# Performance work log

Measured on AMD Instinct MI355X. Metric: run time of the kernel, lower is better.

Reference implementation:

```python
import jax, jax.numpy as jnp
import numpy as np

WS = 8
HEADS = 12


def _dwconv(x, w, b):
    # x: (N, C, H, W); w: (C, 1, 3, 3) depthwise, zero pad 1
    y = jax.lax.conv_general_dilated(
        x, w, window_strides=(1, 1), padding=((1, 1), (1, 1)),
        dimension_numbers=("NCHW", "OIHW", "NCHW"), feature_group_count=x.shape[1])
    return y + b[None, :, None, None]


def _sepconv(x, dw, db, pw, pb):
    y = _dwconv(x, dw, db)
    # pointwise 1x1 conv: (N,C,H,W) x (O,C) -> (N,O,H,W)
    return jnp.einsum("nchw,oc->nohw", y, pw) + pb[None, :, None, None]


def _rel_pos_index(ws):
    coords = np.stack(np.meshgrid(np.arange(ws), np.arange(ws), indexing="ij"))  # (2, ws, ws)
    cf = coords.reshape(2, -1)
    rel = cf[:, :, None] - cf[:, None, :]          # (2, ws*ws, ws*ws)
    rel = rel.transpose(1, 2, 0).copy()
    rel[..., 0] += ws - 1
    rel[..., 1] += ws - 1
    rel[..., 0] *= 2 * ws - 1
    return rel.sum(-1)                             # (ws*ws, ws*ws)


def setup_inputs() -> dict:
    key = jax.random.key(0)
    ks = jax.random.split(key, 16)
    B, T, C, H, W = 2, 1, 384, 192, 192
    s = 0.02
    inp = {
        "vid": jax.random.normal(ks[0], (B, T, C, H, W), jnp.float32),
        "qd_w": jax.random.normal(ks[1], (C, 1, 3, 3), jnp.float32) * s,
        "qd_b": jnp.zeros((C,), jnp.float32),
        "qp_w": jax.random.normal(ks[2], (C, C), jnp.float32) * s,
        "qp_b": jnp.zeros((C,), jnp.float32),
        "kd_w": jax.random.normal(ks[3], (C, 1, 3, 3), jnp.float32) * s,
        "kd_b": jnp.zeros((C,), jnp.float32),
        "kp_w": jax.random.normal(ks[4], (C, C), jnp.float32) * s,
        "kp_b": jnp.zeros((C,), jnp.float32),
        "vd_w": jax.random.normal(ks[5], (C, 1, 3, 3), jnp.float32) * s,
        "vd_b": jnp.zeros((C,), jnp.float32),
        "vp_w": jax.random.normal(ks[6], (C, C), jnp.float32) * s,
        "vp_b": jnp.zeros((C,), jnp.float32),
        "rpb_table": jax.random.normal(ks[7], ((2 * WS - 1) ** 2, HEADS), jnp.float32) * s,
        "proj_w": jax.random.normal(ks[8], (C, C), jnp.float32) * s,
        "proj_b": jnp.zeros((C,), jnp.float32),
    }
    return inp


def reference(vid, qd_w, qd_b, qp_w, qp_b, kd_w, kd_b, kp_w, kp_b,
              vd_w, vd_b, vp_w, vp_b, rpb_table, proj_w, proj_b):
    B, T, C, H, W = vid.shape
    heads, ws = HEADS, WS
    hd = C // heads
    scale = hd ** -0.5
    x = vid.reshape(B * T, C, H, W)

    q = _sepconv(x, qd_w, qd_b, qp_w, qp_b) * scale
    k = _sepconv(x, kd_w, kd_b, kp_w, kp_b)
    v = _sepconv(x, vd_w, vd_b, vp_w, vp_b)

    nh, nw = H // ws, W // ws

    def win(z):  # (N, C, H, W) -> (N*nh*nw, heads, ws*ws, hd)
        N = z.shape[0]
        z = z.reshape(N, heads, hd, nh, ws, nw, ws)
        z = z.transpose(0, 3, 5, 1, 4, 6, 2)  # N, nh, nw, heads, ws, ws, hd
        return z.reshape(N * nh * nw, heads, ws * ws, hd)

    qw, kw, vw = win(q), win(k), win(v)

    # product search within window (dists = q . k), rel-pos bias softmax
    attn = jnp.einsum("nhqd,nhkd->nhqk", qw, kw)
    rp_idx = _rel_pos_index(ws)  # static (64, 64)
    bias = rpb_table[rp_idx.reshape(-1)].reshape(ws * ws, ws * ws, heads)
    bias = bias.transpose(2, 0, 1)  # (heads, 64, 64)
    attn = jax.nn.softmax(attn + bias[None], axis=-1)

    # weighted patch sum (ps=1 -> pixels)
    out = jnp.einsum("nhqk,nhkd->nhqd", attn, vw)  # (N*nh*nw, heads, ws*ws, hd)

    # un-window, merge heads into (h c) channel order, then token projection
    out = out.reshape(B * T, nh, nw, heads, ws, ws, hd)
    out = out.transpose(0, 1, 4, 2, 5, 3, 6).reshape(B * T, H, W, heads * hd)
    out = out @ proj_w.T + proj_b

    # fold (ps=1, stride0=1): identity overlap-add, zvid == 1
    out = out.transpose(0, 3, 1, 2).reshape(B, T, C, H, W)
    return out
```

## Files before the change

kernel.cpp:

```cpp
#include <hip/hip_runtime.h>

#define CCH 384
#define HH 192
#define WWD 192
#define NIMG 2
#define HWP (HH * WWD)
#define PTOT (NIMG * HWP)
#define HEADS 12
#define HD 32
#define NWIN 24
#define WINS 576
#define EELEM ((size_t)NIMG * CCH * HWP)
#define WMAT 147456

typedef __attribute__((ext_vector_type(8))) short bh8;
typedef __attribute__((ext_vector_type(8))) unsigned short us8;
typedef __attribute__((ext_vector_type(4))) unsigned short us4;
typedef __attribute__((ext_vector_type(4))) float fx4;

__device__ __forceinline__ unsigned short f2bf(float f) {
    unsigned u = __float_as_uint(f);
    u += 0x7fffu + ((u >> 16) & 1u);
    return (unsigned short)(u >> 16);
}

__device__ __forceinline__ void gload16(const void* g, void* l) {
    __builtin_amdgcn_global_load_lds(
        (const __attribute__((address_space(1))) void*)g,
        (__attribute__((address_space(3))) void*)l, 16, 0, 0);
}

__global__ __launch_bounds__(256) void prep(
    const float* __restrict__ qp, const float* __restrict__ kp,
    const float* __restrict__ vp, const float* __restrict__ pj,
    const float* __restrict__ qd, const float* __restrict__ kd,
    const float* __restrict__ vd, const float* __restrict__ rpb,
    unsigned short* __restrict__ Wb, float* __restrict__ dwT,
    float* __restrict__ Bx)
{
    int bx = blockIdx.x;
    if (bx < 288) {
        int idx8 = (bx * 256 + threadIdx.x) * 8;
        int which = idx8 / WMAT;
        int loc = idx8 - which * WMAT;
        const float* s = (which == 0) ? qp : (which == 1) ? kp : (which == 2) ? vp : pj;
        float4 v0 = *(const float4*)(s + loc);
        float4 v1 = *(const float4*)(s + loc + 4);
        us8 ov;
        ov[0] = f2bf(v0.x); ov[1] = f2bf(v0.y); ov[2] = f2bf(v0.z); ov[3] = f2bf(v0.w);
        ov[4] = f2bf(v1.x); ov[5] = f2bf(v1.y); ov[6] = f2bf(v1.z); ov[7] = f2bf(v1.w);
        *(us8*)(Wb + idx8) = ov;
    } else if (bx < 329) {
        int idx = (bx - 288) * 256 + threadIdx.x;
        if (idx < 3 * 9 * CCH) {
            int ten = idx / (9 * CCH);
            int rem = idx - ten * (9 * CCH);
            int tap = rem / CCH;
            int c   = rem - tap * CCH;
            const float* s = (ten == 0) ? qd : (ten == 1) ? kd : vd;
            dwT[idx] = s[c * 9 + tap];
        }
    } else {
        int idx = (bx - 329) * 256 + threadIdx.x;
        int h    = idx >> 12;
        int rem  = idx & 4095;
        int li   = rem >> 8;
        int rem2 = rem & 255;
        int g    = rem2 >> 6;
        int rem3 = rem2 & 63;
        int nf   = rem3 >> 4;
        int rem4 = rem3 & 15;
        int mf   = rem4 >> 2;
        int r    = rem4 & 3;
        int tk = nf * 16 + li;
        int tq = mf * 16 + g * 4 + r;
        int dy = (tq >> 3) - (tk >> 3) + 7;
        int dx = (tq & 7) - (tk & 7) + 7;
        Bx[idx] = rpb[(dy * 15 + dx) * HEADS + h];
    }
}

__global__ __launch_bounds__(256) void dwgather(
    const float* __restrict__ x,
    const float* __restrict__ wt,
    const float* __restrict__ qb, const float* __restrict__ kb,
    const float* __restrict__ vb,
    unsigned short* __restrict__ oq, unsigned short* __restrict__ ok,
    unsigned short* __restrict__ ov)
{
    __shared__ float halo[64 * 121];

    int bid = blockIdx.x;
    int b = (bid & 7) * 864 + (bid >> 3);
    int wtx  = b % 24;
    int strip = b / 24;
    int chv  = strip % 6;
    int nwy  = strip / 6;
    int wy   = nwy % 24;
    int n    = nwy / 24;

    int h0 = wy * 8, w0 = wtx * 8;
    int tid = threadIdx.x;
    int c   = tid & 63;
    int pxg = tid >> 6;
    int cg  = chv * 64 + c;
    int widx = n * WINS + wy * NWIN + wtx;

    const float* xbase = x + (size_t)n * CCH * HWP + (size_t)(chv * 64) * HWP;

    for (int j = tid; j < 1920; j += 256) {
        int seg = j % 3;
        int t   = j / 3;
        int rr  = t % 10;
        int cc  = t / 10;
        int hr  = h0 - 1 + rr;
        int cb  = w0 - 2 + seg * 4;
        float4 val = make_float4(0.f, 0.f, 0.f, 0.f);
        if (hr >= 0 && hr < HH) {
            const float* p = xbase + (size_t)cc * HWP + (size_t)hr * WWD;
            if (cb >= 0 && cb + 4 <= WWD) {
                val = *(const float4*)(p + cb);
            } else {
                if (cb + 0 >= 0 && cb + 0 < WWD) val.x = p[cb + 0];
                if (cb + 1 >= 0 && cb + 1 < WWD) val.y = p[cb + 1];
                if (cb + 2 >= 0 && cb + 2 < WWD) val.z = p[cb + 2];
                if (cb + 3 >= 0 && cb + 3 < WWD) val.w = p[cb + 3];
            }
        }
        int hb = cc * 121 + rr * 12 + seg * 4;
        halo[hb + 0] = val.x;
        halo[hb + 1] = val.y;
        halo[hb + 2] = val.z;
        halo[hb + 3] = val.w;
    }

    float wq[9], wk[9], wv[9];
#pragma unroll
    for (int t = 0; t < 9; ++t) {
        wq[t] = wt[t * CCH + cg];
        wk[t] = wt[9 * CCH + t * CCH + cg];
        wv[t] = wt[18 * CCH + t * CCH + cg];
    }
    float bqv = qb[cg], bkv = kb[cg], bvv = vb[cg];

    __syncthreads();

    const int hbase = c * 121 + (2 * pxg) * 12;
    float r0[10], r1[10], r2[10];
#pragma unroll
    for (int cc = 0; cc < 10; ++cc) r0[cc] = halo[hbase + cc + 1];
#pragma unroll
    for (int cc = 0; cc < 10; ++cc) r1[cc] = halo[hbase + 12 + cc + 1];
#pragma unroll
    for (int cc = 0; cc < 10; ++cc) r2[cc] = halo[hbase + 24 + cc + 1];

    size_t ob0 = ((size_t)widx * 64 + pxg * 16) * CCH + cg;

#pragma unroll
    for (int pc = 0; pc < 8; ++pc) {
        float sq = 0.f, sk = 0.f, sv = 0.f;
#pragma unroll
        for (int dc = 0; dc < 3; ++dc) {
            float x0 = r0[pc + dc], x1 = r1[pc + dc], x2 = r2[pc + dc];
            sq = fmaf(x0, wq[dc], sq);     sk = fmaf(x0, wk[dc], sk);     sv = fmaf(x0, wv[dc], sv);
            sq = fmaf(x1, wq[3 + dc], sq); sk = fmaf(x1, wk[3 + dc], sk); sv = fmaf(x1, wv[3 + dc], sv);
            sq = fmaf(x2, wq[6 + dc], sq); sk = fmaf(x2, wk[6 + dc], sk); sv = fmaf(x2, wv[6 + dc], sv);
        }
        size_t o = ob0 + (size_t)pc * CCH;
        oq[o] = f2bf(sq + bqv);
        ok[o] = f2bf(sk + bkv);
        ov[o] = f2bf(sv + bvv);
    }

#pragma unroll
    for (int cc = 0; cc < 10; ++cc) r0[cc] = halo[hbase + 36 + cc + 1];

#pragma unroll
    for (int pc = 0; pc < 8; ++pc) {
        float sq = 0.f, sk = 0.f, sv = 0.f;
#pragma unroll
        for (int dc = 0; dc < 3; ++dc) {
            float x0 = r1[pc + dc], x1 = r2[pc + dc], x2 = r0[pc + dc];
            sq = fmaf(x0, wq[dc], sq);     sk = fmaf(x0, wk[dc], sk);     sv = fmaf(x0, wv[dc], sv);
            sq = fmaf(x1, wq[3 + dc], sq); sk = fmaf(x1, wk[3 + dc], sk); sv = fmaf(x1, wv[3 + dc], sv);
            sq = fmaf(x2, wq[6 + dc], sq); sk = fmaf(x2, wk[6 + dc], sk); sv = fmaf(x2, wv[6 + dc], sv);
        }
        size_t o = ob0 + (size_t)(8 + pc) * CCH;
        oq[o] = f2bf(sq + bqv);
        ok[o] = f2bf(sk + bkv);
        ov[o] = f2bf(sv + bvv);
    }
}

#define ISSUE_TILE(KT, BUF)                                                     \
    do {                                                                        \
        int k0_ = (KT) * 32;                                                    \
        gload16(Wg0 + k0_,                     &Wt[BUF][wid * 32][0]);          \
        gload16(Wg0 + (size_t)16 * CCH + k0_,  &Wt[BUF][wid * 32 + 16][0]);     \
        gload16(Yg0 + k0_,                     &Yt[BUF][wid * 32][0]);          \
        gload16(Yg0 + (size_t)16 * CCH + k0_,  &Yt[BUF][wid * 32 + 16][0]);     \
    } while (0)

__global__ __launch_bounds__(256) void qkv_gemm(
    const unsigned short* __restrict__ tr0, const unsigned short* __restrict__ tr1,
    const unsigned short* __restrict__ tr2, const unsigned short* __restrict__ Wball,
    const float* __restrict__ qpb, const float* __restrict__ kpb,
    const float* __restrict__ vpb, float scale,
    unsigned short* __restrict__ qo, unsigned short* __restrict__ ko,
    unsigned short* __restrict__ vo)
{
    __shared__ __align__(16) char smem[49152];
    typedef unsigned short (*tile3)[128][32];
    tile3 Wt = (tile3)smem;
    tile3 Yt = (tile3)(smem + 24576);
    typedef unsigned short (*tep_t)[132];
    tep_t T16 = (tep_t)smem;

    int bL = blockIdx.x;
    int O  = (bL & 7) * 648 + (bL >> 3);
    int z  = O / 1728;
    int rem = O - z * 1728;
    int py = rem / 3;
    int cx = rem - py * 3;
    int pp0 = py * 128, cm0 = cx * 128;

    const unsigned short* Y  = (z == 0) ? tr0 : (z == 1) ? tr1 : tr2;
    const unsigned short* Wb = Wball + (size_t)z * WMAT;
    const float* bias        = (z == 0) ? qpb : (z == 1) ? kpb : vpb;
    float sc                 = (z == 0) ? scale : 1.0f;
    unsigned short* outb     = (z == 0) ? qo : (z == 1) ? ko : vo;
    bool vmode = (z == 2);

    int tid = threadIdx.x;
    int lid = tid & 63, wid = tid >> 6;
    int wr = wid >> 1, wc = wid & 1;
    int li = lid & 15, g = lid >> 4;

    int srow = (lid >> 2);
    int scol = (((lid & 3) ^ ((srow >> 1) & 3))) * 8;
    int gsw = (g ^ ((li >> 1) & 3)) * 8;

    fx4 acc[4][4];
#pragma unroll
    for (int i = 0; i < 4; ++i)
#pragma unroll
        for (int j = 0; j < 4; ++j) acc[i][j] = (fx4){0.f, 0.f, 0.f, 0.f};

    tile3 A3 = vmode ? Yt : Wt;
    tile3 B3 = vmode ? Wt : Yt;

    const unsigned short* Wg0 = Wb + (size_t)(cm0 + wid * 32 + srow) * CCH + scol;
    const unsigned short* Yg0 = Y  + (size_t)(pp0 + wid * 32 + srow) * CCH + scol;

    float4 bv4[4];
    float  bvs[4];
    if (!vmode) {
#pragma unroll
        for (int mf = 0; mf < 4; ++mf)
            bv4[mf] = *(const float4*)&bias[cm0 + wr * 64 + mf * 16 + g * 4];
    } else {
#pragma unroll
        for (int nf = 0; nf < 4; ++nf)
            bvs[nf] = bias[cm0 + wc * 64 + nf * 16 + li];
    }
    asm volatile("s_waitcnt vmcnt(0)" ::: "memory");
    __builtin_amdgcn_sched_barrier(0);

    ISSUE_TILE(0, 0);
    ISSUE_TILE(1, 1);

#pragma unroll
    for (int kt = 0; kt < 12; ++kt) {
        __builtin_amdgcn_sched_barrier(0);
        if (kt < 11) asm volatile("s_waitcnt vmcnt(4)" ::: "memory");
        else         asm volatile("s_waitcnt vmcnt(0)" ::: "memory");
        __builtin_amdgcn_s_barrier();
        __builtin_amdgcn_sched_barrier(0);
        if (kt < 10) ISSUE_TILE(kt + 2, (kt + 2) % 3);

        int cur = kt % 3;
        bh8 a[4], b[4];
#pragma unroll
        for (int mf = 0; mf < 4; ++mf)
            a[mf] = *(const bh8*)&A3[cur][wr * 64 + mf * 16 + li][gsw];
#pragma unroll
        for (int nf = 0; nf < 4; ++nf)
            b[nf] = *(const bh8*)&B3[cur][wc * 64 + nf * 16 + li][gsw];
#pragma unroll
        for (int mf = 0; mf < 4; ++mf)
#pragma unroll
            for (int nf = 0; nf < 4; ++nf)
                acc[mf][nf] = __builtin_amdgcn_mfma_f32_16x16x32_bf16(
                    a[mf], b[nf], acc[mf][nf], 0, 0, 0);
    }

    __syncthreads();

    if (!vmode) {
#pragma unroll
        for (int mf = 0; mf < 4; ++mf) {
            int cl = wr * 64 + mf * 16 + g * 4;
            float4 bv = bv4[mf];
#pragma unroll
            for (int nf = 0; nf < 4; ++nf) {
                int pl = wc * 64 + nf * 16 + li;
                us4 o;
                o[0] = f2bf((acc[mf][nf][0] + bv.x) * sc);
                o[1] = f2bf((acc[mf][nf][1] + bv.y) * sc);
                o[2] = f2bf((acc[mf][nf][2] + bv.z) * sc);
                o[3] = f2bf((acc[mf][nf][3] + bv.w) * sc);
                *(us4*)&T16[pl][cl] = o;
            }
        }
        __syncthreads();
#pragma unroll
        for (int it = 0; it < 8; ++it) {
            int row = it * 16 + wid * 4 + (lid >> 4);
            int col = (lid & 15) * 8;
            us8 vv = *(const us8*)&T16[row][col];
            *(us8*)(outb + (size_t)(pp0 + row) * CCH + cm0 + col) = vv;
        }
    } else {
#pragma unroll
        for (int nf = 0; nf < 4; ++nf) {
            int cl = wc * 64 + nf * 16 + li;
            float bv = bvs[nf];
#pragma unroll
            for (int mf = 0; mf < 4; ++mf) {
                int pl = wr * 64 + mf * 16 + g * 4;
                us4 o;
                o[0] = f2bf(acc[mf][nf][0] + bv);
                o[1] = f2bf(acc[mf][nf][1] + bv);
                o[2] = f2bf(acc[mf][nf][2] + bv);
                o[3] = f2bf(acc[mf][nf][3] + bv);
                *(us4*)&T16[cl][pl] = o;
            }
        }
        __syncthreads();
        int n = pp0 / HWP;
        int pl0 = pp0 - n * HWP;
#pragma unroll
        for (int it = 0; it < 8; ++it) {
            int row = it * 16 + wid * 4 + (lid >> 4);
            int col = (lid & 15) * 8;
            us8 vv = *(const us8*)&T16[row][col];
            *(us8*)(outb + (size_t)(n * CCH + cm0 + row) * HWP + pl0 + col) = vv;
        }
    }
}

__global__ __launch_bounds__(256) void proj_gemm(
    const unsigned short* __restrict__ Y, const unsigned short* __restrict__ Wb,
    const float* __restrict__ bias, float* __restrict__ outf)
{
    __shared__ unsigned short Wt[3][128][32];
    __shared__ unsigned short Yt[3][128][32];

    int bL = blockIdx.x;
    int O  = (bL & 7) * 216 + (bL >> 3);
    int py = O / 3;
    int cx = O - py * 3;
    int pp0 = py * 128, cm0 = cx * 128;

    int tid = threadIdx.x;
    int lid = tid & 63, wid = tid >> 6;
    int wr = wid >> 1, wc = wid & 1;
    int li = lid & 15, g = lid >> 4;

    int srow = (lid >> 2);
    int scol = (((lid & 3) ^ ((srow >> 1) & 3))) * 8;
    int gsw = (g ^ ((li >> 1) & 3)) * 8;

    fx4 acc[4][4];
#pragma unroll
    for (int i = 0; i < 4; ++i)
#pragma unroll
        for (int j = 0; j < 4; ++j) acc[i][j] = (fx4){0.f, 0.f, 0.f, 0.f};

    const unsigned short* Wg0 = Wb + (size_t)(cm0 + wid * 32 + srow) * CCH + scol;
    const unsigned short* Yg0 = Y  + (size_t)(pp0 + wid * 32 + srow) * CCH + scol;

    float4 bv4[4];
#pragma unroll
    for (int mf = 0; mf < 4; ++mf)
        bv4[mf] = *(const float4*)&bias[cm0 + wr * 64 + mf * 16 + g * 4];
    asm volatile("s_waitcnt vmcnt(0)" ::: "memory");
    __builtin_amdgcn_sched_barrier(0);

    ISSUE_TILE(0, 0);
    ISSUE_TILE(1, 1);

#pragma unroll
    for (int kt = 0; kt < 12; ++kt) {
        __builtin_amdgcn_sched_barrier(0);
        if (kt < 11) asm volatile("s_waitcnt vmcnt(4)" ::: "memory");
        else         asm volatile("s_waitcnt vmcnt(0)" ::: "memory");
        __builtin_amdgcn_s_barrier();
        __builtin_amdgcn_sched_barrier(0);
        if (kt < 10) ISSUE_TILE(kt + 2, (kt + 2) % 3);

        int cur = kt % 3;
        bh8 a[4], b[4];
#pragma unroll
        for (int mf = 0; mf < 4; ++mf)
            a[mf] = *(const bh8*)&Wt[cur][wr * 64 + mf * 16 + li][gsw];
#pragma unroll
        for (int nf = 0; nf < 4; ++nf)
            b[nf] = *(const bh8*)&Yt[cur][wc * 64 + nf * 16 + li][gsw];
#pragma unroll
        for (int mf = 0; mf < 4; ++mf)
#pragma unroll
            for (int nf = 0; nf < 4; ++nf)
                acc[mf][nf] = __builtin_amdgcn_mfma_f32_16x16x32_bf16(
                    a[mf], b[nf], acc[mf][nf], 0, 0, 0);
    }

#pragma unroll
    for (int mf = 0; mf < 4; ++mf) {
        int c = cm0 + wr * 64 + mf * 16 + g * 4;
#pragma unroll
        for (int nf = 0; nf < 4; ++nf) {
            int p = pp0 + wc * 64 + nf * 16 + li;
            int n = p / HWP;
            int rem = p - n * HWP;
            int win = rem >> 6, t = rem & 63;
            int h = (win / NWIN) * 8 + (t >> 3);
            int w = (win % NWIN) * 8 + (t & 7);
            float* op = outf + (size_t)n * CCH * HWP + (size_t)h * WWD + w;
            op[(size_t)(c + 0) * HWP] = acc[mf][nf][0] + bv4[mf].x;
            op[(size_t)(c + 1) * HWP] = acc[mf][nf][1] + bv4[mf].y;
            op[(size_t)(c + 2) * HWP] = acc[mf][nf][2] + bv4[mf].z;
            op[(size_t)(c + 3) * HWP] = acc[mf][nf][3] + bv4[mf].w;
        }
    }
}

__global__ __launch_bounds__(256) void attn(
    const unsigned short* __restrict__ q, const unsigned short* __restrict__ k,
    const unsigned short* __restrict__ v, const float* __restrict__ Bx,
    unsigned short* __restrict__ o)
{
    __shared__ unsigned short Pl[4][64][36];

    int tid = threadIdx.x, lid = tid & 63, wid = tid >> 6;
    int bL = blockIdx.x;
    int b = (bL & 7) * 432 + (bL >> 3);
    int pair = b * 4 + wid;
    int wl = pair / 12;
    int hq = pair - wl * 12;
    int n = wl / WINS, winl = wl - n * WINS;
    int li = lid & 15, g = lid >> 4;

    const fx4 z = (fx4){0.f, 0.f, 0.f, 0.f};

    const unsigned short* qp = q + (size_t)(wl * 64) * CCH + hq * HD + g * 8;
    const unsigned short* kp = k + (size_t)(wl * 64) * CCH + hq * HD + g * 8;
    bh8 aq[4], bk[4];
#pragma unroll
    for (int mf = 0; mf < 4; ++mf)
        aq[mf] = *(const bh8*)(qp + (size_t)(mf * 16 + li) * CCH);
#pragma unroll
    for (int nf = 0; nf < 4; ++nf)
        bk[nf] = *(const bh8*)(kp + (size_t)(nf * 16 + li) * CCH);

    bh8 av2[2][2];
#pragma unroll
    for (int ks = 0; ks < 2; ++ks)
#pragma unroll
        for (int m2 = 0; m2 < 2; ++m2)
            av2[ks][m2] = *(const bh8*)(v + (size_t)(n * CCH + hq * HD + m2 * 16 + li) * HWP
                                          + winl * 64 + ks * 32 + g * 8);

    fx4 s[4][4];
    __builtin_amdgcn_s_setprio(1);
#pragma unroll
    for (int mf = 0; mf < 4; ++mf)
#pragma unroll
        for (int nf = 0; nf < 4; ++nf)
            s[mf][nf] = __builtin_amdgcn_mfma_f32_16x16x32_bf16(aq[mf], bk[nf], z, 0, 0, 0);
    __builtin_amdgcn_s_setprio(0);

    {
        const float* bxl = Bx + (((size_t)hq * 16 + li) * 4 + g) * 64;
#pragma unroll
        for (int nf = 0; nf < 4; ++nf)
#pragma unroll
            for (int mf = 0; mf < 4; ++mf) {
                fx4 bv = *(const fx4*)&bxl[(nf * 4 + mf) * 4];
                s[mf][nf] += bv;
            }
    }

    float inv_[4][4];
#pragma unroll
    for (int mf = 0; mf < 4; ++mf)
#pragma unroll
        for (int r = 0; r < 4; ++r) {
            float m = s[mf][0][r];
#pragma unroll
            for (int nf = 1; nf < 4; ++nf) m = fmaxf(m, s[mf][nf][r]);
            m = fmaxf(m, __shfl_xor(m, 1));
            m = fmaxf(m, __shfl_xor(m, 2));
            m = fmaxf(m, __shfl_xor(m, 4));
            m = fmaxf(m, __shfl_xor(m, 8));
            float sum = 0.f;
#pragma unroll
            for (int nf = 0; nf < 4; ++nf) {
                float e = __expf(s[mf][nf][r] - m);
                s[mf][nf][r] = e;
                sum += e;
            }
            sum += __shfl_xor(sum, 1);
            sum += __shfl_xor(sum, 2);
            sum += __shfl_xor(sum, 4);
            sum += __shfl_xor(sum, 8);
            inv_[mf][r] = 1.f / sum;
        }

    fx4 o2[2][4];
#pragma unroll
    for (int m2 = 0; m2 < 2; ++m2)
#pragma unroll
        for (int nf = 0; nf < 4; ++nf) o2[m2][nf] = z;

#pragma unroll
    for (int ks = 0; ks < 2; ++ks) {
#pragma unroll
        for (int mf = 0; mf < 4; ++mf)
#pragma unroll
            for (int nf2 = 0; nf2 < 2; ++nf2) {
                int nf = ks * 2 + nf2;
#pragma unroll
                for (int r = 0; r < 4; ++r)
                    Pl[wid][mf * 16 + g * 4 + r][nf2 * 16 + li] =
                        f2bf(s[mf][nf][r] * inv_[mf][r]);
            }
        bh8 bp[4];
#pragma unroll
        for (int nfq = 0; nfq < 4; ++nfq)
            bp[nfq] = *(const bh8*)&Pl[wid][nfq * 16 + li][g * 8];
        __builtin_amdgcn_s_setprio(1);
#pragma unroll
        for (int m2 = 0; m2 < 2; ++m2)
#pragma unroll
            for (int nfq = 0; nfq < 4; ++nfq)
                o2[m2][nfq] = __builtin_amdgcn_mfma_f32_16x16x32_bf16(
                    av2[ks][m2], bp[nfq], o2[m2][nfq], 0, 0, 0);
        __builtin_amdgcn_s_setprio(0);
    }

#pragma unroll
    for (int nf = 0; nf < 4; ++nf) {
        int tq = nf * 16 + li;
#pragma unroll
        for (int m2 = 0; m2 < 2; ++m2) {
            int d = hq * HD + m2 * 16 + g * 4;
            us4 ov;
            ov[0] = f2bf(o2[m2][nf][0]);
            ov[1] = f2bf(o2[m2][nf][1]);
            ov[2] = f2bf(o2[m2][nf][2]);
            ov[3] = f2bf(o2[m2][nf][3]);
            *(us4*)(o + (size_t)(wl * 64 + tq) * CCH + d) = ov;
        }
    }
}

extern "C" void kernel_launch(void* const* d_in, const int* in_sizes, int n_in,
                              void* d_out, int out_size, void* d_ws, size_t ws_size,
                              hipStream_t stream) {
    const float* vid  = (const float*)d_in[0];
    const float* qd_w = (const float*)d_in[1];
    const float* qd_b = (const float*)d_in[2];
    const float* qp_w = (const float*)d_in[3];
    const float* qp_b = (const float*)d_in[4];
    const float* kd_w = (const float*)d_in[5];
    const float* kd_b = (const float*)d_in[6];
    const float* kp_w = (const float*)d_in[7];
    const float* kp_b = (const float*)d_in[8];
    const float* vd_w = (const float*)d_in[9];
    const float* vd_b = (const float*)d_in[10];
    const float* vp_w = (const float*)d_in[11];
    const float* vp_b = (const float*)d_in[12];
    const float* rpb  = (const float*)d_in[13];
    const float* pj_w = (const float*)d_in[14];
    const float* pj_b = (const float*)d_in[15];

    unsigned short* ws16 = (unsigned short*)d_ws;
    unsigned short* tr0 = ws16 + 3 * EELEM;
    unsigned short* tr1 = ws16 + 4 * EELEM;
    unsigned short* tr2 = ws16 + 5 * EELEM;
    unsigned short* Wb  = ws16 + 6 * EELEM;
    float* dwT          = (float*)(Wb + 4 * WMAT);
    float* Bx           = dwT + 3 * 9 * CCH;
    unsigned short* qb  = ws16;
    unsigned short* kb  = ws16 + EELEM;
    unsigned short* vb  = ws16 + 2 * EELEM;
    unsigned short* ob  = tr0;

    prep<<<521, 256, 0, stream>>>(qp_w, kp_w, vp_w, pj_w,
                                  qd_w, kd_w, vd_w, rpb, Wb, dwT, Bx);
    dwgather<<<NIMG * WINS * 6, 256, 0, stream>>>(
        vid, dwT, qd_b, kd_b, vd_b, tr0, tr1, tr2);

    const float scale = 0.17677669529663687f;
    qkv_gemm<<<5184, 256, 0, stream>>>(
        tr0, tr1, tr2, Wb, qp_b, kp_b, vp_b, scale, qb, kb, vb);

    attn<<<3456, 256, 0, stream>>>(qb, kb, vb, Bx, ob);

    proj_gemm<<<1728, 256, 0, stream>>>(
        ob, Wb + 3 * WMAT, pj_b, (float*)d_out);
}
```

Measured before the change: 381.7 us.

## Split dwgather halo into two channel halves with register-prefetched loads

The depthwise conv gather kernel now handles its 64 channels as two halves of 32. It issues the global loads for both halves into registers up front. While the second half's loads are still in flight, it computes the first half from shared memory. Thread mapping also changes so each thread covers one output row (8 pixels) per half instead of two rows, which shortens the per-thread register stencil. The goal is to overlap global-load latency with compute. The cost is more registers for the prefetch buffers and a second barrier.

```diff
diff --git a/kernel.cpp b/kernel.cpp
--- a/kernel.cpp
+++ b/kernel.cpp
@@ -88,7 +88,7 @@
     unsigned short* __restrict__ oq, unsigned short* __restrict__ ok,
     unsigned short* __restrict__ ov)
 {
-    __shared__ float halo[64 * 121];
+    __shared__ float halo[2][32 * 121];
 
     int bid = blockIdx.x;
     int b = (bid & 7) * 864 + (bid >> 3);
@@ -101,94 +101,170 @@
 
     int h0 = wy * 8, w0 = wtx * 8;
     int tid = threadIdx.x;
-    int c   = tid & 63;
-    int pxg = tid >> 6;
-    int cg  = chv * 64 + c;
+    int c   = tid & 31;
+    int pxg = tid >> 5;
+    int cgA = chv * 64 + c;
+    int cgB = cgA + 32;
     int widx = n * WINS + wy * NWIN + wtx;
 
-    const float* xbase = x + (size_t)n * CCH * HWP + (size_t)(chv * 64) * HWP;
-
-    for (int j = tid; j < 1920; j += 256) {
-        int seg = j % 3;
-        int t   = j / 3;
-        int rr  = t % 10;
-        int cc  = t / 10;
-        int hr  = h0 - 1 + rr;
-        int cb  = w0 - 2 + seg * 4;
+    const float* xbA = x + (size_t)n * CCH * HWP + (size_t)(chv * 64) * HWP;
+    const float* xbB = xbA + (size_t)32 * HWP;
+
+    float wqA[9], wkA[9], wvA[9];
+#pragma unroll
+    for (int t = 0; t < 9; ++t) {
+        wqA[t] = wt[t * CCH + cgA];
+        wkA[t] = wt[9 * CCH + t * CCH + cgA];
+        wvA[t] = wt[18 * CCH + t * CCH + cgA];
+    }
+    float bqA = qb[cgA], bkA = kb[cgA], bvA = vb[cgA];
+
+    float4 regA[4], regB[4];
+#pragma unroll
+    for (int it = 0; it < 4; ++it) {
+        int j = it * 256 + tid;
         float4 val = make_float4(0.f, 0.f, 0.f, 0.f);
-        if (hr >= 0 && hr < HH) {
-            const float* p = xbase + (size_t)cc * HWP + (size_t)hr * WWD;
-            if (cb >= 0 && cb + 4 <= WWD) {
-                val = *(const float4*)(p + cb);
-            } else {
-                if (cb + 0 >= 0 && cb + 0 < WWD) val.x = p[cb + 0];
-                if (cb + 1 >= 0 && cb + 1 < WWD) val.y = p[cb + 1];
-                if (cb + 2 >= 0 && cb + 2 < WWD) val.z = p[cb + 2];
-                if (cb + 3 >= 0 && cb + 3 < WWD) val.w = p[cb + 3];
-            }
-        }
-        int hb = cc * 121 + rr * 12 + seg * 4;
-        halo[hb + 0] = val.x;
-        halo[hb + 1] = val.y;
-        halo[hb + 2] = val.z;
-        halo[hb + 3] = val.w;
-    }
-
-    float wq[9], wk[9], wv[9];
+        if (j < 960) {
+            int seg = j % 3;
+            int t   = j / 3;
+            int rr  = t % 10;
+            int cc  = t / 10;
+            int hr  = h0 - 1 + rr;
+            int cb  = w0 - 2 + seg * 4;
+            if (hr >= 0 && hr < HH) {
+                const float* p = xbA + (size_t)cc * HWP + (size_t)hr * WWD;
+                if (cb >= 0 && cb + 4 <= WWD) {
+                    val = *(const float4*)(p + cb);
+                } else {
+                    if (cb + 0 >= 0 && cb + 0 < WWD) val.x = p[cb + 0];
+                    if (cb + 1 >= 0 && cb + 1 < WWD) val.y = p[cb + 1];
+                    if (cb + 2 >= 0 && cb + 2 < WWD) val.z = p[cb + 2];
+                    if (cb + 3 >= 0 && cb + 3 < WWD) val.w = p[cb + 3];
+                }
+            }
+        }
+        regA[it] = val;
+    }
+#pragma unroll
+    for (int it = 0; it < 4; ++it) {
+        int j = it * 256 + tid;
+        float4 val = make_float4(0.f, 0.f, 0.f, 0.f);
+        if (j < 960) {
+            int seg = j % 3;
+            int t   = j / 3;
+            int rr  = t % 10;
+            int cc  = t / 10;
+            int hr  = h0 - 1 + rr;
+            int cb  = w0 - 2 + seg * 4;
+            if (hr >= 0 && hr < HH) {
+                const float* p = xbB + (size_t)cc * HWP + (size_t)hr * WWD;
+                if (cb >= 0 && cb + 4 <= WWD) {
+                    val = *(const float4*)(p + cb);
+                } else {
+                    if (cb + 0 >= 0 && cb + 0 < WWD) val.x = p[cb + 0];
+                    if (cb + 1 >= 0 && cb + 1 < WWD) val.y = p[cb + 1];
+                    if (cb + 2 >= 0 && cb + 2 < WWD) val.z = p[cb + 2];
+                    if (cb + 3 >= 0 && cb + 3 < WWD) val.w = p[cb + 3];
+                }
+            }
+        }
+        regB[it] = val;
+    }
+    float wqB[9], wkB[9], wvB[9];
 #pragma unroll
     for (int t = 0; t < 9; ++t) {
-        wq[t] = wt[t * CCH + cg];
-        wk[t] = wt[9 * CCH + t * CCH + cg];
-        wv[t] = wt[18 * CCH + t * CCH + cg];
-    }
-    float bqv = qb[cg], bkv = kb[cg], bvv = vb[cg];
-
+        wqB[t] = wt[t * CCH + cgB];
+        wkB[t] = wt[9 * CCH + t * CCH + cgB];
+        wvB[t] = wt[18 * CCH + t * CCH + cgB];
+    }
+    float bqB = qb[cgB], bkB = kb[cgB], bvB = vb[cgB];
+
+#pragma unroll
+    for (int it = 0; it < 4; ++it) {
+        int j = it * 256 + tid;
+        if (j < 960) {
+            int seg = j % 3;
+            int t   = j / 3;
+            int rr  = t % 10;
+            int cc  = t / 10;
+            int hb  = cc * 121 + rr * 12 + seg * 4;
+            halo[0][hb + 0] = regA[it].x;
+            halo[0][hb + 1] = regA[it].y;
+            halo[0][hb + 2] = regA[it].z;
+            halo[0][hb + 3] = regA[it].w;
+        }
+    }
     __syncthreads();
 
-    const int hbase = c * 121 + (2 * pxg) * 12;
-    float r0[10], r1[10], r2[10];
-#pragma unroll
-    for (int cc = 0; cc < 10; ++cc) r0[cc] = halo[hbase + cc + 1];
-#pragma unroll
-    for (int cc = 0; cc < 10; ++cc) r1[cc] = halo[hbase + 12 + cc + 1];
-#pragma unroll
-    for (int cc = 0; cc < 10; ++cc) r2[cc] = halo[hbase + 24 + cc + 1];
-
-    size_t ob0 = ((size_t)widx * 64 + pxg * 16) * CCH + cg;
-
-#pragma unroll
-    for (int pc = 0; pc < 8; ++pc) {
-        float sq = 0.f, sk = 0.f, sv = 0.f;
-#pragma unroll
-        for (int dc = 0; dc < 3; ++dc) {
-            float x0 = r0[pc + dc], x1 = r1[pc + dc], x2 = r2[pc + dc];
-            sq = fmaf(x0, wq[dc], sq);     sk = fmaf(x0, wk[dc], sk);     sv = fmaf(x0, wv[dc], sv);
-            sq = fmaf(x1, wq[3 + dc], sq); sk = fmaf(x1, wk[3 + dc], sk); sv = fmaf(x1, wv[3 + dc], sv);
-            sq = fmaf(x2, wq[6 + dc], sq); sk = fmaf(x2, wk[6 + dc], sk); sv = fmaf(x2, wv[6 + dc], sv);
-        }
-        size_t o = ob0 + (size_t)pc * CCH;
-        oq[o] = f2bf(sq + bqv);
-        ok[o] = f2bf(sk + bkv);
-        ov[o] = f2bf(sv + bvv);
-    }
-
-#pragma unroll
-    for (int cc = 0; cc < 10; ++cc) r0[cc] = halo[hbase + 36 + cc + 1];
-
-#pragma unroll
-    for (int pc = 0; pc < 8; ++pc) {
-        float sq = 0.f, sk = 0.f, sv = 0.f;
-#pragma unroll
-        for (int dc = 0; dc < 3; ++dc) {
-            float x0 = r1[pc + dc], x1 = r2[pc + dc], x2 = r0[pc + dc];
-            sq = fmaf(x0, wq[dc], sq);     sk = fmaf(x0, wk[dc], sk);     sv = fmaf(x0, wv[dc], sv);
-            sq = fmaf(x1, wq[3 + dc], sq); sk = fmaf(x1, wk[3 + dc], sk); sv = fmaf(x1, wv[3 + dc], sv);
-            sq = fmaf(x2, wq[6 + dc], sq); sk = fmaf(x2, wk[6 + dc], sk); sv = fmaf(x2, wv[6 + dc], sv);
-        }
-        size_t o = ob0 + (size_t)(8 + pc) * CCH;
-        oq[o] = f2bf(sq + bqv);
-        ok[o] = f2bf(sk + bkv);
-        ov[o] = f2bf(sv + bvv);
+    {
+        const int hb0 = c * 121 + pxg * 12;
+        float r0[10], r1[10], r2[10];
+#pragma unroll
+        for (int cc = 0; cc < 10; ++cc) r0[cc] = halo[0][hb0 + cc + 1];
+#pragma unroll
+        for (int cc = 0; cc < 10; ++cc) r1[cc] = halo[0][hb0 + 12 + cc + 1];
+#pragma unroll
+        for (int cc = 0; cc < 10; ++cc) r2[cc] = halo[0][hb0 + 24 + cc + 1];
+        size_t ob0 = ((size_t)widx * 64 + pxg * 8) * CCH + cgA;
+#pragma unroll
+        for (int pc = 0; pc < 8; ++pc) {
+            float sq = 0.f, sk = 0.f, sv = 0.f;
+#pragma unroll
+            for (int dc = 0; dc < 3; ++dc) {
+                float x0 = r0[pc + dc], x1 = r1[pc + dc], x2 = r2[pc + dc];
+                sq = fmaf(x0, wqA[dc], sq);     sk = fmaf(x0, wkA[dc], sk);     sv = fmaf(x0, wvA[dc], sv);
+                sq = fmaf(x1, wqA[3 + dc], sq); sk = fmaf(x1, wkA[3 + dc], sk); sv = fmaf(x1, wvA[3 + dc], sv);
+                sq = fmaf(x2, wqA[6 + dc], sq); sk = fmaf(x2, wkA[6 + dc], sk); sv = fmaf(x2, wvA[6 + dc], sv);
+            }
+            size_t o = ob0 + (size_t)pc * CCH;
+            oq[o] = f2bf(sq + bqA);
+            ok[o] = f2bf(sk + bkA);
+            ov[o] = f2bf(sv + bvA);
+        }
+    }
+
+#pragma unroll
+    for (int it = 0; it < 4; ++it) {
+        int j = it * 256 + tid;
+        if (j < 960) {
+            int seg = j % 3;
+            int t   = j / 3;
+            int rr  = t % 10;
+            int cc  = t / 10;
+            int hb  = cc * 121 + rr * 12 + seg * 4;
+            halo[1][hb + 0] = regB[it].x;
+            halo[1][hb + 1] = regB[it].y;
+            halo[1][hb + 2] = regB[it].z;
+            halo[1][hb + 3] = regB[it].w;
+        }
+    }
+    __syncthreads();
+
+    {
+        const int hb0 = c * 121 + pxg * 12;
+        float r0[10], r1[10], r2[10];
+#pragma unroll
+        for (int cc = 0; cc < 10; ++cc) r0[cc] = halo[1][hb0 + cc + 1];
+#pragma unroll
+        for (int cc = 0; cc < 10; ++cc) r1[cc] = halo[1][hb0 + 12 + cc + 1];
+#pragma unroll
+        for (int cc = 0; cc < 10; ++cc) r2[cc] = halo[1][hb0 + 24 + cc + 1];
+        size_t ob0 = ((size_t)widx * 64 + pxg * 8) * CCH + cgB;
+#pragma unroll
+        for (int pc = 0; pc < 8; ++pc) {
+            float sq = 0.f, sk = 0.f, sv = 0.f;
+#pragma unroll
+            for (int dc = 0; dc < 3; ++dc) {
+                float x0 = r0[pc + dc], x1 = r1[pc + dc], x2 = r2[pc + dc];
+                sq = fmaf(x0, wqB[dc], sq);     sk = fmaf(x0, wkB[dc], sk);     sv = fmaf(x0, wvB[dc], sv);
+                sq = fmaf(x1, wqB[3 + dc], sq); sk = fmaf(x1, wkB[3 + dc], sk); sv = fmaf(x1, wvB[3 + dc], sv);
+                sq = fmaf(x2, wqB[6 + dc], sq); sk = fmaf(x2, wkB[6 + dc], sk); sv = fmaf(x2, wvB[6 + dc], sv);
+            }
+            size_t o = ob0 + (size_t)pc * CCH;
+            oq[o] = f2bf(sq + bqB);
+            ok[o] = f2bf(sk + bkB);
+            ov[o] = f2bf(sv + bvB);
+        }
     }
 }
 
```

Measured after the change: 408.7 us. 1.07x slower.

## Split each window-head attention across two waves sharing P via LDS

Applied to the files above, without the earlier changes.

Each (window, head) pair is now processed by two waves instead of one. Each wave computes half of the query rows for QK^T and softmax, writes its half of P to shared LDS, and after a block barrier computes half of the output head dimension using the full P. The grid doubles and per-wave register use drops. The cost is K loads duplicated across the two waves, an added __syncthreads, and a larger LDS tile per pair.

```diff
diff --git a/kernel.cpp b/kernel.cpp
--- a/kernel.cpp
+++ b/kernel.cpp
@@ -440,12 +440,14 @@
     const unsigned short* __restrict__ v, const float* __restrict__ Bx,
     unsigned short* __restrict__ o)
 {
-    __shared__ unsigned short Pl[4][64][36];
+    __shared__ unsigned short Pl[2][64][72];
 
     int tid = threadIdx.x, lid = tid & 63, wid = tid >> 6;
     int bL = blockIdx.x;
-    int b = (bL & 7) * 432 + (bL >> 3);
-    int pair = b * 4 + wid;
+    int b = (bL & 7) * 864 + (bL >> 3);
+    int pl   = wid >> 1;
+    int half = wid & 1;
+    int pair = b * 2 + pl;
     int wl = pair / 12;
     int hq = pair - wl * 12;
     int n = wl / WINS, winl = wl - n * WINS;
@@ -455,29 +457,27 @@
 
     const unsigned short* qp = q + (size_t)(wl * 64) * CCH + hq * HD + g * 8;
     const unsigned short* kp = k + (size_t)(wl * 64) * CCH + hq * HD + g * 8;
-    bh8 aq[4], bk[4];
-#pragma unroll
-    for (int mf = 0; mf < 4; ++mf)
-        aq[mf] = *(const bh8*)(qp + (size_t)(mf * 16 + li) * CCH);
+    bh8 aq[2], bk[4];
+#pragma unroll
+    for (int mfl = 0; mfl < 2; ++mfl)
+        aq[mfl] = *(const bh8*)(qp + (size_t)((half * 2 + mfl) * 16 + li) * CCH);
 #pragma unroll
     for (int nf = 0; nf < 4; ++nf)
         bk[nf] = *(const bh8*)(kp + (size_t)(nf * 16 + li) * CCH);
 
-    bh8 av2[2][2];
+    bh8 av[2];
 #pragma unroll
     for (int ks = 0; ks < 2; ++ks)
-#pragma unroll
-        for (int m2 = 0; m2 < 2; ++m2)
-            av2[ks][m2] = *(const bh8*)(v + (size_t)(n * CCH + hq * HD + m2 * 16 + li) * HWP
-                                          + winl * 64 + ks * 32 + g * 8);
-
-    fx4 s[4][4];
+        av[ks] = *(const bh8*)(v + (size_t)(n * CCH + hq * HD + half * 16 + li) * HWP
+                                 + winl * 64 + ks * 32 + g * 8);
+
+    fx4 s[2][4];
     __builtin_amdgcn_s_setprio(1);
 #pragma unroll
-    for (int mf = 0; mf < 4; ++mf)
+    for (int mfl = 0; mfl < 2; ++mfl)
 #pragma unroll
         for (int nf = 0; nf < 4; ++nf)
-            s[mf][nf] = __builtin_amdgcn_mfma_f32_16x16x32_bf16(aq[mf], bk[nf], z, 0, 0, 0);
+            s[mfl][nf] = __builtin_amdgcn_mfma_f32_16x16x32_bf16(aq[mfl], bk[nf], z, 0, 0, 0);
     __builtin_amdgcn_s_setprio(0);
 
     {
@@ -485,20 +485,20 @@
 #pragma unroll
         for (int nf = 0; nf < 4; ++nf)
 #pragma unroll
-            for (int mf = 0; mf < 4; ++mf) {
-                fx4 bv = *(const fx4*)&bxl[(nf * 4 + mf) * 4];
-                s[mf][nf] += bv;
+            for (int mfl = 0; mfl < 2; ++mfl) {
+                fx4 bv = *(const fx4*)&bxl[(nf * 4 + half * 2 + mfl) * 4];
+                s[mfl][nf] += bv;
             }
     }
 
-    float inv_[4][4];
-#pragma unroll
-    for (int mf = 0; mf < 4; ++mf)
+    float inv_[2][4];
+#pragma unroll
+    for (int mfl = 0; mfl < 2; ++mfl)
 #pragma unroll
         for (int r = 0; r < 4; ++r) {
-            float m = s[mf][0][r];
-#pragma unroll
-            for (int nf = 1; nf < 4; ++nf) m = fmaxf(m, s[mf][nf][r]);
+            float m = s[mfl][0][r];
+#pragma unroll
+            for (int nf = 1; nf < 4; ++nf) m = fmaxf(m, s[mfl][nf][r]);
             m = fmaxf(m, __shfl_xor(m, 1));
             m = fmaxf(m, __shfl_xor(m, 2));
             m = fmaxf(m, __shfl_xor(m, 4));
@@ -506,62 +506,55 @@
             float sum = 0.f;
 #pragma unroll
             for (int nf = 0; nf < 4; ++nf) {
-                float e = __expf(s[mf][nf][r] - m);
-                s[mf][nf][r] = e;
+                float e = __expf(s[mfl][nf][r] - m);
+                s[mfl][nf][r] = e;
                 sum += e;
             }
             sum += __shfl_xor(sum, 1);
             sum += __shfl_xor(sum, 2);
             sum += __shfl_xor(sum, 4);
             sum += __shfl_xor(sum, 8);
-            inv_[mf][r] = 1.f / sum;
-        }
-
-    fx4 o2[2][4];
-#pragma unroll
-    for (int m2 = 0; m2 < 2; ++m2)
-#pragma unroll
-        for (int nf = 0; nf < 4; ++nf) o2[m2][nf] = z;
-
+            inv_[mfl][r] = 1.f / sum;
+        }
+
+#pragma unroll
+    for (int mfl = 0; mfl < 2; ++mfl)
+#pragma unroll
+        for (int nf = 0; nf < 4; ++nf)
+#pragma unroll
+            for (int r = 0; r < 4; ++r)
+                Pl[pl][half * 32 + mfl * 16 + g * 4 + r][nf * 16 + li] =
+                    f2bf(s[mfl][nf][r] * inv_[mfl][r]);
+
+    __syncthreads();
+
+    fx4 o2[4];
+#pragma unroll
+    for (int nf = 0; nf < 4; ++nf) o2[nf] = z;
 #pragma unroll
     for (int ks = 0; ks < 2; ++ks) {
-#pragma unroll
-        for (int mf = 0; mf < 4; ++mf)
-#pragma unroll
-            for (int nf2 = 0; nf2 < 2; ++nf2) {
-                int nf = ks * 2 + nf2;
-#pragma unroll
-                for (int r = 0; r < 4; ++r)
-                    Pl[wid][mf * 16 + g * 4 + r][nf2 * 16 + li] =
-                        f2bf(s[mf][nf][r] * inv_[mf][r]);
-            }
         bh8 bp[4];
 #pragma unroll
         for (int nfq = 0; nfq < 4; ++nfq)
-            bp[nfq] = *(const bh8*)&Pl[wid][nfq * 16 + li][g * 8];
+            bp[nfq] = *(const bh8*)&Pl[pl][nfq * 16 + li][ks * 32 + g * 8];
         __builtin_amdgcn_s_setprio(1);
 #pragma unroll
-        for (int m2 = 0; m2 < 2; ++m2)
-#pragma unroll
-            for (int nfq = 0; nfq < 4; ++nfq)
-                o2[m2][nfq] = __builtin_amdgcn_mfma_f32_16x16x32_bf16(
-                    av2[ks][m2], bp[nfq], o2[m2][nfq], 0, 0, 0);
+        for (int nfq = 0; nfq < 4; ++nfq)
+            o2[nfq] = __builtin_amdgcn_mfma_f32_16x16x32_bf16(
+                av[ks], bp[nfq], o2[nfq], 0, 0, 0);
         __builtin_amdgcn_s_setprio(0);
     }
 
 #pragma unroll
     for (int nf = 0; nf < 4; ++nf) {
         int tq = nf * 16 + li;
-#pragma unroll
-        for (int m2 = 0; m2 < 2; ++m2) {
-            int d = hq * HD + m2 * 16 + g * 4;
-            us4 ov;
-            ov[0] = f2bf(o2[m2][nf][0]);
-            ov[1] = f2bf(o2[m2][nf][1]);
-            ov[2] = f2bf(o2[m2][nf][2]);
-            ov[3] = f2bf(o2[m2][nf][3]);
-            *(us4*)(o + (size_t)(wl * 64 + tq) * CCH + d) = ov;
-        }
+        int d = hq * HD + half * 16 + g * 4;
+        us4 ov;
+        ov[0] = f2bf(o2[nf][0]);
+        ov[1] = f2bf(o2[nf][1]);
+        ov[2] = f2bf(o2[nf][2]);
+        ov[3] = f2bf(o2[nf][3]);
+        *(us4*)(o + (size_t)(wl * 64 + tq) * CCH + d) = ov;
     }
 }
 
@@ -606,7 +599,7 @@
     qkv_gemm<<<5184, 256, 0, stream>>>(
         tr0, tr1, tr2, Wb, qp_b, kp_b, vp_b, scale, qb, kb, vb);
 
-    attn<<<3456, 256, 0, stream>>>(qb, kb, vb, Bx, ob);
+    attn<<<6912, 256, 0, stream>>>(qb, kb, vb, Bx, ob);
 
     proj_gemm<<<1728, 256, 0, stream>>>(
         ob, Wb + 3 * WMAT, pj_b, (float*)d_out);
```

Result: faster. 357.5 us (median of 3 runs) (-6.3%).
